# Kernel tuning notes

Hardware: AMD Instinct MI355X
Metric: run time of the kernel (lower is better)

Reference implementation:

```python
import jax, jax.numpy as jnp
import numpy as np

B, L, H, A, M, E, R = 4, 1024, 1024, 16, 128, 32, 992
EMB, BLK, C = 768, 64, 97


def setup_inputs() -> dict:
    key = jax.random.key(0)
    ks = jax.random.split(key, 8)
    return {
        'seq_lhs': jax.random.normal(ks[0], (B, L, H), jnp.float32),
        'ent_lhs': jax.random.normal(ks[1], (B, M, H), jnp.float32),
        'ent_to_seq_attn': jax.random.uniform(ks[2], (B, A, M, L), jnp.float32),
        'mention_entity_ids': jax.random.randint(ks[3], (B, M), 0, E, jnp.int32),
        'hts': jax.random.randint(ks[4], (B, R, 2), 0, E, jnp.int32),
        'head_W': jax.random.normal(ks[5], (2 * H, EMB), jnp.float32) * 0.02,
        'head_b': jnp.zeros((EMB,), jnp.float32),
        'tail_W': jax.random.normal(ks[6], (2 * H, EMB), jnp.float32) * 0.02,
        'tail_b': jnp.zeros((EMB,), jnp.float32),
        'bil_W': jax.random.normal(ks[7], (EMB * BLK, C), jnp.float32) * 0.02,
        'bil_b': jnp.zeros((C,), jnp.float32),
    }


def _pool_doc(seq, ents, attn, ids, ht):
    # seq [L,H], ents [M,H], attn [A,M,L], ids [M], ht [R,2]
    counts = jax.ops.segment_sum(jnp.ones((M,), seq.dtype), ids, num_segments=E)  # [E]
    nz = counts > 0
    # stable segment logsumexp over mentions of each entity (matches torch.logsumexp;
    # single-mention entities reduce to the raw embedding, empty entities -> zeros)
    mx = jax.ops.segment_max(ents, ids, num_segments=E)              # [E,H]
    mx = jnp.where(nz[:, None], mx, 0.0)
    s = jax.ops.segment_sum(jnp.exp(ents - mx[ids]), ids, num_segments=E)
    s = jnp.where(nz[:, None], s, 1.0)
    ent_emb = jnp.where(nz[:, None], mx + jnp.log(s), 0.0)           # [E,H]
    # mean of mention->seq attention per entity (empty -> zeros)
    attn_m = jnp.transpose(attn, (1, 0, 2))                          # [M,A,L]
    asum = jax.ops.segment_sum(attn_m, ids, num_segments=E)          # [E,A,L]
    ent_attn = jnp.where(nz[:, None, None], asum / jnp.maximum(counts, 1.0)[:, None, None], 0.0)
    # gather head/tail entities for each pair
    hs, ts = ent_emb[ht[:, 0]], ent_emb[ht[:, 1]]                    # [R,H]
    ha, ta = ent_attn[ht[:, 0]], ent_attn[ht[:, 1]]                  # [R,A,L]
    w = (ha * ta).mean(axis=1)                                       # [R,L]
    w = w / (w.sum(axis=1, keepdims=True) + 1e-5)
    rel = jnp.einsum('ld,rl->rd', seq, w)                            # [R,H]
    return hs, ts, rel


def reference(seq_lhs, ent_lhs, ent_to_seq_attn, mention_entity_ids, hts,
              head_W, head_b, tail_W, tail_b, bil_W, bil_b):
    hs, ts, rel = jax.vmap(_pool_doc)(seq_lhs, ent_lhs, ent_to_seq_attn,
                                      mention_entity_ids, hts)
    hs = hs.reshape(-1, H)
    ts = ts.reshape(-1, H)
    rel = rel.reshape(-1, H)
    hs = jnp.tanh(jnp.concatenate([hs, rel], axis=1) @ head_W + head_b)  # [N,EMB]
    ts = jnp.tanh(jnp.concatenate([ts, rel], axis=1) @ tail_W + tail_b)
    b1 = hs.reshape(-1, EMB // BLK, BLK)
    b2 = ts.reshape(-1, EMB // BLK, BLK)
    bl = (b1[:, :, :, None] * b2[:, :, None, :]).reshape(-1, EMB * BLK)  # [N,EMB*BLK]
    return bl @ bil_W + bil_b                                            # [N,C]
```

## Files before the change

kernel.cpp:

```cpp
#include <hip/hip_runtime.h>
#include <hip/hip_bf16.h>
#include <math.h>

constexpr int cB   = 4;
constexpr int cL   = 1024;
constexpr int cH   = 1024;
constexpr int cA   = 16;
constexpr int cM   = 128;
constexpr int cE   = 32;
constexpr int cR   = 992;
constexpr int cEMB = 768;
constexpr int cC   = 97;
constexpr int cN   = cB * cR;
constexpr int cNG  = 8;

typedef unsigned short ushort;
typedef __attribute__((ext_vector_type(4))) unsigned short ushort4v;
typedef __attribute__((ext_vector_type(8))) short short8;
typedef __attribute__((ext_vector_type(4))) float float4v;

static __device__ inline float bf2f(ushort u) {
    unsigned v = ((unsigned)u) << 16;
    float f;
    __builtin_memcpy(&f, &v, 4);
    return f;
}
static __device__ inline ushort f2bf(float f) {
    unsigned u;
    __builtin_memcpy(&u, &f, 4);
    unsigned r = (u + 0x7FFFu + ((u >> 16) & 1u)) >> 16;
    return (ushort)r;
}

static __device__ inline void gld16(const ushort* src, ushort* dstbase) {
    __builtin_amdgcn_global_load_lds(
        (const __attribute__((address_space(1))) unsigned int*)src,
        (__attribute__((address_space(3))) unsigned int*)dstbase, 16, 0, 0);
}

__global__ void prep_k(const float* __restrict__ bil_W,
                       const float* __restrict__ head_W,
                       const float* __restrict__ tail_W,
                       const float* __restrict__ seq_lhs,
                       const float* __restrict__ ent_lhs,
                       const int* __restrict__ ids,
                       ushort* __restrict__ Wf,
                       ushort* __restrict__ WTh, ushort* __restrict__ WTt,
                       ushort* __restrict__ seqT,
                       ushort* __restrict__ ent_bf, int* __restrict__ counts) {
    const int id = blockIdx.x;
    const int tid = threadIdx.x;
    __shared__ float tile[32][33];
    __shared__ ushort sWb[64 * 136];
    __shared__ int sid[cM];

    if (id < 768) {
        const int si = id;
        for (int idx = tid; idx < 64 * 128; idx += 256) {
            int r = idx >> 7, c = idx & 127;
            float v = (c < cC) ? bil_W[((size_t)si * 64 + r) * cC + c] : 0.f;
            sWb[r * 136 + c] = f2bf(v);
        }
        __syncthreads();
#pragma unroll
        for (int p = 0; p < 4; p++) {
            int e = tid + p * 256;
            int f = e >> 6, lane = e & 63;
            int g = lane >> 4, col = lane & 15;
            int khalf = f >> 3, ct = f & 7;
            int jb = khalf * 32 + g * 8;
            int c = ct * 16 + col;
            short8 v;
#pragma unroll
            for (int jj = 0; jj < 8; jj++) v[jj] = (short)sWb[(jb + jj) * 136 + c];
            *(short8*)&Wf[(((size_t)si * 16 + f) * 64 + lane) * 8] = v;
        }
    } else if (id < 3840) {
        const int t = id - 768;
        const int bx = t & 63, by = (t >> 6) % 24, bz = t / 1536;
        const float* src = bz ? tail_W : head_W;
        ushort* dst = bz ? WTt : WTh;
        int r0 = bx * 32, c0 = by * 32;
        int tx = tid & 31, ty = tid >> 5;
        for (int p = 0; p < 4; p++) {
            int r = r0 + ty + p * 8, c = c0 + tx;
            tile[ty + p * 8][tx] = src[(size_t)r * cEMB + c];
        }
        __syncthreads();
        for (int p = 0; p < 4; p++) {
            int c = c0 + ty + p * 8, r = r0 + tx;
            dst[(size_t)c * (2 * cH) + r] = f2bf(tile[tx][ty + p * 8]);
        }
    } else if (id < 7936) {
        const int t = id - 3840;
        const int bx = t & 31, by = (t >> 5) & 31, z = t >> 10;
        int r0 = bx * 32, c0 = by * 32;
        int tx = tid & 31, ty = tid >> 5;
        for (int p = 0; p < 4; p++) {
            int r = r0 + ty + p * 8, c = c0 + tx;
            tile[ty + p * 8][tx] = seq_lhs[((size_t)z * cL + r) * cH + c];
        }
        __syncthreads();
        for (int p = 0; p < 4; p++) {
            int c = c0 + ty + p * 8, r = r0 + tx;
            seqT[((size_t)z * cH + c) * cL + r] = f2bf(tile[tx][ty + p * 8]);
        }
    } else {
        const int t = id - 7936;
        const int e = t & 31, b = (t >> 5) & 3, z = t >> 7;
        if (tid < cM) sid[tid] = ids[b * cM + tid];
        __syncthreads();
        int cnt = 0;
        for (int m = 0; m < cM; m++) cnt += (sid[m] == e) ? 1 : 0;
        if (z == 0 && tid == 0) counts[b * cE + e] = cnt;
        int h = z * 256 + tid;
        float mx = -1e30f;
        for (int m = 0; m < cM; m++)
            if (sid[m] == e) mx = fmaxf(mx, ent_lhs[(size_t)(b * cM + m) * cH + h]);
        float s = 0.f;
        for (int m = 0; m < cM; m++)
            if (sid[m] == e) s += __expf(ent_lhs[(size_t)(b * cM + m) * cH + h] - mx);
        ent_bf[(size_t)(b * cE + e) * cH + h] = f2bf((cnt > 0) ? (mx + __logf(s)) : 0.f);
    }
}

__global__ void ent_attn_k(const float* __restrict__ attn, const int* __restrict__ ids,
                           const int* __restrict__ counts, ushort* __restrict__ ent_attn) {
    int ba = blockIdx.x;
    int b = ba / cA, a = ba % cA;
    int tid = threadIdx.x;
    int l = blockIdx.y * 256 + tid;
    __shared__ int sid[cM];
    __shared__ int scnt[cE];
    __shared__ float sacc[256 * 33];
    if (tid < cM) sid[tid] = ids[b * cM + tid];
    if (tid < cE) scnt[tid] = counts[b * cE + tid];
    float* acc = &sacc[tid * 33];
    for (int e2 = 0; e2 < cE; e2++) acc[e2] = 0.f;
    __syncthreads();
    const float* ap = attn + ((size_t)(b * cA + a) * cM) * cL + l;
    for (int m = 0; m < cM; m++) acc[sid[m]] += ap[(size_t)m * cL];
    for (int e2 = 0; e2 < cE; e2++) {
        ent_attn[((size_t)(b * cE + e2) * cA + a) * cL + l] =
            f2bf(acc[e2] / (float)max(scnt[e2], 1));
    }
}

__global__ void w_k(const ushort* __restrict__ ent_attn, const int* __restrict__ hts,
                    ushort* __restrict__ w) {
    int nr = blockIdx.x;
    int b = nr / cR;
    int he = hts[nr * 2 + 0], te = hts[nr * 2 + 1];
    int tid = threadIdx.x;
    int l0 = tid * 4;
    const ushort* ha = ent_attn + ((size_t)(b * cE + he) * cA) * cL + l0;
    const ushort* ta = ent_attn + ((size_t)(b * cE + te) * cA) * cL + l0;
    float v[4] = {0.f, 0.f, 0.f, 0.f};
#pragma unroll
    for (int a = 0; a < cA; a++) {
        ushort4v hv = *(const ushort4v*)&ha[(size_t)a * cL];
        ushort4v tv = *(const ushort4v*)&ta[(size_t)a * cL];
#pragma unroll
        for (int i = 0; i < 4; i++) v[i] += bf2f(hv[i]) * bf2f(tv[i]);
    }
    float psum = 0.f;
#pragma unroll
    for (int i = 0; i < 4; i++) { v[i] *= (1.0f / cA); psum += v[i]; }
    for (int off = 32; off > 0; off >>= 1) psum += __shfl_down(psum, off, 64);
    __shared__ float red[4];
    if ((tid & 63) == 0) red[tid >> 6] = psum;
    __syncthreads();
    float tot = red[0] + red[1] + red[2] + red[3];
    float inv = 1.0f / (tot + 1e-5f);
    ushort4v o;
#pragma unroll
    for (int i = 0; i < 4; i++) o[i] = f2bf(v[i] * inv);
    *(ushort4v*)&w[(size_t)nr * cL + l0] = o;
}

__global__ __launch_bounds__(256) void
rel_mfma2_k(const ushort* __restrict__ wbf, const ushort* __restrict__ seqT,
            ushort* __restrict__ relbf) {
    const int b = blockIdx.z;
    const int h0 = blockIdx.x * 128, r0 = blockIdx.y * 64;
    const int tid = threadIdx.x, lane = tid & 63, wv = tid >> 6;
    const int col = lane & 15, g4 = lane >> 4;
    const int wr = wv >> 1, wc = wv & 1;

    __shared__ ushort sA[2][64 * 64];
    __shared__ ushort sB[2][128 * 64];

    const int lr = lane >> 3;
    const int swz = (lane & 7) ^ lr;

    const int ra0 = wv * 8 + lr, ra1 = ra0 + 32;
    const ushort* a0p = wbf + ((size_t)b * cR + min(r0 + ra0, cR - 1)) * cL + swz * 8;
    const ushort* a1p = wbf + ((size_t)b * cR + min(r0 + ra1, cR - 1)) * cL + swz * 8;
    const ushort* bptr[4];
#pragma unroll
    for (int p = 0; p < 4; p++)
        bptr[p] = seqT + ((size_t)b * cH + h0 + p * 32 + wv * 8 + lr) * cL + swz * 8;

    float4v acc[2][4];
#pragma unroll
    for (int mt = 0; mt < 2; mt++)
#pragma unroll
        for (int ct = 0; ct < 4; ct++) acc[mt][ct] = (float4v){0.f, 0.f, 0.f, 0.f};

#define REL_STAGE(kt, buf) {                                                   \
        gld16(a0p + (kt), &sA[buf][wv * 512]);                                 \
        gld16(a1p + (kt), &sA[buf][(4 + wv) * 512]);                           \
        _Pragma("unroll")                                                      \
        for (int p = 0; p < 4; p++)                                            \
            gld16(bptr[p] + (kt), &sB[buf][(p * 4 + wv) * 512]);               \
    }

    REL_STAGE(0, 0);
    __syncthreads();
    int cur = 0;
    for (int kt = 0; kt < cL; kt += 64) {
        if (kt + 64 < cL) REL_STAGE(kt + 64, cur ^ 1);
#pragma unroll
        for (int k0 = 0; k0 < 64; k0 += 32) {
            short8 av[2];
#pragma unroll
            for (int mt = 0; mt < 2; mt++) {
                int ra = wr * 32 + mt * 16 + col;
                int sg = ((k0 >> 3) + g4) ^ (ra & 7);
                av[mt] = *(const short8*)&sA[cur][ra * 64 + sg * 8];
            }
#pragma unroll
            for (int ct = 0; ct < 4; ct++) {
                int rb = wc * 64 + ct * 16 + col;
                int sg = ((k0 >> 3) + g4) ^ (rb & 7);
                short8 bv = *(const short8*)&sB[cur][rb * 64 + sg * 8];
#pragma unroll
                for (int mt = 0; mt < 2; mt++)
                    acc[mt][ct] = __builtin_amdgcn_mfma_f32_16x16x32_bf16(
                        av[mt], bv, acc[mt][ct], 0, 0, 0);
            }
        }
        __syncthreads();
        cur ^= 1;
    }
#undef REL_STAGE

#pragma unroll
    for (int mt = 0; mt < 2; mt++) {
#pragma unroll
        for (int ct = 0; ct < 4; ct++) {
            int h = h0 + wc * 64 + ct * 16 + col;
            int rowb = r0 + wr * 32 + mt * 16 + g4 * 4;
#pragma unroll
            for (int reg = 0; reg < 4; reg++) {
                int r = rowb + reg;
                if (r < cR)
                    relbf[((size_t)b * cR + r) * cH + h] = f2bf(acc[mt][ct][reg]);
            }
        }
    }
}

__global__ __launch_bounds__(256) void
proj_mfma3_k(const ushort* __restrict__ ent_bf, const ushort* __restrict__ relbf,
             const int* __restrict__ hts,
             const ushort* __restrict__ WTh, const ushort* __restrict__ WTt,
             const float* __restrict__ head_b, const float* __restrict__ tail_b,
             ushort* __restrict__ hsp, ushort* __restrict__ tsp) {
    const int sel = blockIdx.z;
    const ushort* WTp = sel ? WTt : WTh;
    const float* bias = sel ? tail_b : head_b;
    ushort* outp = sel ? tsp : hsp;

    const int e0 = blockIdx.x * 128, n0 = blockIdx.y * 64;
    const int tid = threadIdx.x, lane = tid & 63, wv = tid >> 6;
    const int col = lane & 15, g4 = lane >> 4;
    const int wr = wv >> 1, wc = wv & 1;

    __shared__ ushort sA[2][64 * 64];
    __shared__ ushort sB[2][128 * 64];

    const int lr = lane >> 3;
    const int swz = (lane & 7) ^ lr;

    const int ra0 = wv * 8 + lr, ra1 = ra0 + 32;
    size_t eb0, eb1;
    { int n = n0 + ra0, bb = n / cR; eb0 = ((size_t)(bb * cE + hts[n * 2 + sel])) * cH; }
    { int n = n0 + ra1, bb = n / cR; eb1 = ((size_t)(bb * cE + hts[n * 2 + sel])) * cH; }
    const ushort* aent0 = ent_bf + eb0 + swz * 8;
    const ushort* aent1 = ent_bf + eb1 + swz * 8;
    const ushort* arel0 = relbf + (size_t)(n0 + ra0) * cH + swz * 8;
    const ushort* arel1 = relbf + (size_t)(n0 + ra1) * cH + swz * 8;

    const ushort* bptr[4];
#pragma unroll
    for (int p = 0; p < 4; p++)
        bptr[p] = WTp + (size_t)(e0 + p * 32 + wv * 8 + lr) * (2 * cH) + swz * 8;

    float4v acc[2][4];
#pragma unroll
    for (int mt = 0; mt < 2; mt++)
#pragma unroll
        for (int ct = 0; ct < 4; ct++) acc[mt][ct] = (float4v){0.f, 0.f, 0.f, 0.f};

#define PROJ_STAGE(kt, buf) {                                                  \
        const ushort* a0 = ((kt) < cH) ? aent0 + (kt) : arel0 + ((kt) - cH);   \
        const ushort* a1 = ((kt) < cH) ? aent1 + (kt) : arel1 + ((kt) - cH);   \
        gld16(a0, &sA[buf][wv * 512]);                                         \
        gld16(a1, &sA[buf][(4 + wv) * 512]);                                   \
        _Pragma("unroll")                                                      \
        for (int p = 0; p < 4; p++)                                            \
            gld16(bptr[p] + (kt), &sB[buf][(p * 4 + wv) * 512]);               \
    }

    PROJ_STAGE(0, 0);
    __syncthreads();
    int cur = 0;
    for (int kt = 0; kt < 2 * cH; kt += 64) {
        if (kt + 64 < 2 * cH) PROJ_STAGE(kt + 64, cur ^ 1);
#pragma unroll
        for (int k0 = 0; k0 < 64; k0 += 32) {
            short8 av[2];
#pragma unroll
            for (int mt = 0; mt < 2; mt++) {
                int ra = wr * 32 + mt * 16 + col;
                int sg = ((k0 >> 3) + g4) ^ (ra & 7);
                av[mt] = *(const short8*)&sA[cur][ra * 64 + sg * 8];
            }
#pragma unroll
            for (int ct = 0; ct < 4; ct++) {
                int rb = wc * 64 + ct * 16 + col;
                int sg = ((k0 >> 3) + g4) ^ (rb & 7);
                short8 bv = *(const short8*)&sB[cur][rb * 64 + sg * 8];
#pragma unroll
                for (int mt = 0; mt < 2; mt++)
                    acc[mt][ct] = __builtin_amdgcn_mfma_f32_16x16x32_bf16(
                        av[mt], bv, acc[mt][ct], 0, 0, 0);
            }
        }
        __syncthreads();
        cur ^= 1;
    }
#undef PROJ_STAGE

#pragma unroll
    for (int mt = 0; mt < 2; mt++) {
#pragma unroll
        for (int ct = 0; ct < 4; ct++) {
            int e = e0 + wc * 64 + ct * 16 + col;
            float bv = bias[e];
            int rowb = n0 + wr * 32 + mt * 16 + g4 * 4;
#pragma unroll
            for (int reg = 0; reg < 4; reg++)
                outp[(size_t)(rowb + reg) * cEMB + e] = f2bf(tanhf(acc[mt][ct][reg] + bv));
        }
    }
}

__global__ __launch_bounds__(256) void
bil_mfma13_k(const ushort* __restrict__ hsp, const ushort* __restrict__ tsp,
             const ushort* __restrict__ Wf, float* __restrict__ part) {
    const int grp = blockIdx.x;
    const int n0 = blockIdx.y * 64;
    const int tid = threadIdx.x;
    const int lane = tid & 63, wv = tid >> 6;
    const int col = lane & 15, g4 = lane >> 4;

    __shared__ float sHs[32 * 68];

    float4v acc[4][2];
#pragma unroll
    for (int mt = 0; mt < 4; mt++)
#pragma unroll
        for (int ctl = 0; ctl < 2; ctl++) acc[mt][ctl] = (float4v){0.f, 0.f, 0.f, 0.f};

    const float4v kZero = {0.f, 0.f, 0.f, 0.f};

    const ushort* WfG = Wf + (size_t)grp * 3 * 32 * 8192;
    const ushort* wbase = WfG + ((size_t)(wv * 2) * 64 + lane) * 8;

#define WLOAD(dst, t) {                                                        \
        const ushort* _p = wbase + (size_t)(t) * 8192;                         \
        dst[0][0] = *(const short8*)&_p[0];                                    \
        dst[0][1] = *(const short8*)&_p[512];                                  \
        dst[1][0] = *(const short8*)&_p[4096];                                 \
        dst[1][1] = *(const short8*)&_p[4608];                                 \
    }

#define BILSTEP(ii, w) {                                                       \
        float4v hsv[4];                                                        \
        _Pragma("unroll")                                                      \
        for (int mt = 0; mt < 4; mt++)                                         \
            hsv[mt] = *(const float4v*)&sHs[(ii) * 68 + mt * 16 + g4 * 4];     \
        _Pragma("unroll")                                                      \
        for (int ctl = 0; ctl < 2; ctl++) {                                    \
            _Pragma("unroll")                                                  \
            for (int mt = 0; mt < 4; mt++) {                                   \
                float4v P = __builtin_amdgcn_mfma_f32_16x16x32_bf16(           \
                    tsA[mt][0], w[0][ctl], kZero, 0, 0, 0);                    \
                P = __builtin_amdgcn_mfma_f32_16x16x32_bf16(                   \
                    tsA[mt][1], w[1][ctl], P, 0, 0, 0);                        \
                acc[mt][ctl] += hsv[mt] * P;                                   \
            }                                                                  \
        }                                                                      \
    }

    short8 tsA[4][2];
    short8 wA[2][2], wB[2][2];
    WLOAD(wA, 0);

    for (int s = 0; s < 3; ++s) {
        const int islice = grp * 3 + s;
        const int kb = islice >> 1;

        __syncthreads();
        {
            int row = tid & 63, seg = tid >> 6;
            short8 v = *(const short8*)
                &hsp[(size_t)(n0 + row) * cEMB + islice * 32 + seg * 8];
#pragma unroll
            for (int jj = 0; jj < 8; jj++)
                sHs[(seg * 8 + jj) * 68 + row] = bf2f((ushort)v[jj]);
        }
#pragma unroll
        for (int mt = 0; mt < 4; mt++)
#pragma unroll
            for (int kh = 0; kh < 2; kh++)
                tsA[mt][kh] = *(const short8*)
                    &tsp[(size_t)(n0 + mt * 16 + col) * cEMB
                         + kb * 64 + kh * 32 + g4 * 8];
        __syncthreads();

        for (int i = 0; i < 32; i += 2) {
            const int t = s * 32 + i;
            WLOAD(wB, t + 1);
            BILSTEP(i, wA);
            if (t + 2 < 96) WLOAD(wA, t + 2);
            BILSTEP(i + 1, wB);
        }
    }
#undef WLOAD
#undef BILSTEP

    float* pbase = part + (size_t)grp * cN * 128;
#pragma unroll
    for (int mt = 0; mt < 4; mt++) {
#pragma unroll
        for (int ctl = 0; ctl < 2; ctl++) {
            int c = (wv * 2 + ctl) * 16 + col;
            int rowb = n0 + mt * 16 + g4 * 4;
#pragma unroll
            for (int reg = 0; reg < 4; reg++)
                pbase[(size_t)(rowb + reg) * 128 + c] = acc[mt][ctl][reg];
        }
    }
}

__global__ void bil_reduce_k(const float* __restrict__ part,
                             const float* __restrict__ bil_b,
                             float* __restrict__ out) {
    int n = blockIdx.x;
    int c = threadIdx.x;
    if (c >= cC) return;
    float s = bil_b[c];
#pragma unroll
    for (int g = 0; g < cNG; g++)
        s += part[((size_t)g * cN + n) * 128 + c];
    out[(size_t)n * cC + c] = s;
}

extern "C" void kernel_launch(void* const* d_in, const int* in_sizes, int n_in,
                              void* d_out, int out_size, void* d_ws, size_t ws_size,
                              hipStream_t stream) {
    const float* seq_lhs  = (const float*)d_in[0];
    const float* ent_lhs  = (const float*)d_in[1];
    const float* attn     = (const float*)d_in[2];
    const int*   ids      = (const int*)d_in[3];
    const int*   hts      = (const int*)d_in[4];
    const float* head_W   = (const float*)d_in[5];
    const float* head_b   = (const float*)d_in[6];
    const float* tail_W   = (const float*)d_in[7];
    const float* tail_b   = (const float*)d_in[8];
    const float* bil_W    = (const float*)d_in[9];
    const float* bil_b    = (const float*)d_in[10];
    float* out = (float*)d_out;

    char* ws = (char*)d_ws;
    int*    counts   = (int*)(ws + 0);
    ushort* ent_bf   = (ushort*)(ws + 512);
    ushort* ent_attn = (ushort*)(ws + 262656);
    ushort* wbuf     = (ushort*)(ws + 4456960);
    ushort* relbf    = (ushort*)(ws + 12583424);
    ushort* hsp      = (ushort*)(ws + 20709888);
    ushort* tsp      = (ushort*)(ws + 26804736);
    ushort* Wf       = (ushort*)(ws + 32899584);
    ushort* WTh      = (ushort*)(ws + 45482496);
    ushort* WTt      = (ushort*)(ws + 48628224);
    ushort* seqT     = (ushort*)(ws + 51773952);
    float*  part     = (float*)(ws + 262656);

    hipLaunchKernelGGL(prep_k, dim3(8448), dim3(256), 0, stream,
                       bil_W, head_W, tail_W, seq_lhs, ent_lhs, ids,
                       Wf, WTh, WTt, seqT, ent_bf, counts);
    hipLaunchKernelGGL(ent_attn_k, dim3(cB * cA, cL / 256), dim3(256), 0, stream,
                       attn, ids, counts, ent_attn);
    hipLaunchKernelGGL(w_k, dim3(cN), dim3(256), 0, stream,
                       ent_attn, hts, wbuf);
    hipLaunchKernelGGL(rel_mfma2_k, dim3(cH / 128, 16, cB), dim3(256), 0, stream,
                       wbuf, seqT, relbf);
    hipLaunchKernelGGL(proj_mfma3_k, dim3(cEMB / 128, cN / 64, 2), dim3(256), 0, stream,
                       ent_bf, relbf, hts, WTh, WTt, head_b, tail_b, hsp, tsp);
    hipLaunchKernelGGL(bil_mfma13_k, dim3(cNG, cN / 64), dim3(256), 0, stream,
                       hsp, tsp, Wf, part);
    hipLaunchKernelGGL(bil_reduce_k, dim3(cN), dim3(128), 0, stream,
                       part, bil_b, out);
}
```

Before: 296.3 us.

## Stream bilinear weights through a per-wave LDS ring buffer with async loads

```diff
diff --git a/kernel.cpp b/kernel.cpp
--- a/kernel.cpp
+++ b/kernel.cpp
@@ -358,7 +358,7 @@
 }
 
 __global__ __launch_bounds__(256) void
-bil_mfma13_k(const ushort* __restrict__ hsp, const ushort* __restrict__ tsp,
+bil_mfma15_k(const ushort* __restrict__ hsp, const ushort* __restrict__ tsp,
              const ushort* __restrict__ Wf, float* __restrict__ part) {
     const int grp = blockIdx.x;
     const int n0 = blockIdx.y * 64;
@@ -367,6 +367,7 @@
     const int col = lane & 15, g4 = lane >> 4;
 
     __shared__ float sHs[32 * 68];
+    __shared__ ushort sWr[4][4][2048];
 
     float4v acc[4][2];
 #pragma unroll
@@ -377,37 +378,46 @@
     const float4v kZero = {0.f, 0.f, 0.f, 0.f};
 
     const ushort* WfG = Wf + (size_t)grp * 3 * 32 * 8192;
-    const ushort* wbase = WfG + ((size_t)(wv * 2) * 64 + lane) * 8;
-
-#define WLOAD(dst, t) {                                                        \
-        const ushort* _p = wbase + (size_t)(t) * 8192;                         \
-        dst[0][0] = *(const short8*)&_p[0];                                    \
-        dst[0][1] = *(const short8*)&_p[512];                                  \
-        dst[1][0] = *(const short8*)&_p[4096];                                 \
-        dst[1][1] = *(const short8*)&_p[4608];                                 \
-    }
-
-#define BILSTEP(ii, w) {                                                       \
+    const ushort* srcb = WfG + ((size_t)(wv * 2) * 64 + lane) * 8;
+
+#define WSTAGE(tt, slot) {                                                     \
+        const ushort* _s = srcb + (size_t)(tt) * 8192;                         \
+        gld16(_s,        &sWr[wv][slot][0]);                                   \
+        gld16(_s + 512,  &sWr[wv][slot][512]);                                 \
+        gld16(_s + 4096, &sWr[wv][slot][1024]);                                \
+        gld16(_s + 4608, &sWr[wv][slot][1536]);                                \
+    }
+
+#define BILSTEP15(ii, slot) {                                                  \
+        const ushort* _w = &sWr[wv][slot][lane * 8];                           \
+        short8 w00 = *(const short8*)&_w[0];                     \
+        short8 w01 = *(const short8*)&_w[512];                   \
+        short8 w10 = *(const short8*)&_w[1024];                  \
+        short8 w11 = *(const short8*)&_w[1536];                  \
         float4v hsv[4];                                                        \
         _Pragma("unroll")                                                      \
         for (int mt = 0; mt < 4; mt++)                                         \
             hsv[mt] = *(const float4v*)&sHs[(ii) * 68 + mt * 16 + g4 * 4];     \
         _Pragma("unroll")                                                      \
-        for (int ctl = 0; ctl < 2; ctl++) {                                    \
-            _Pragma("unroll")                                                  \
-            for (int mt = 0; mt < 4; mt++) {                                   \
-                float4v P = __builtin_amdgcn_mfma_f32_16x16x32_bf16(           \
-                    tsA[mt][0], w[0][ctl], kZero, 0, 0, 0);                    \
-                P = __builtin_amdgcn_mfma_f32_16x16x32_bf16(                   \
-                    tsA[mt][1], w[1][ctl], P, 0, 0, 0);                        \
-                acc[mt][ctl] += hsv[mt] * P;                                   \
-            }                                                                  \
+        for (int mt = 0; mt < 4; mt++) {                                       \
+            float4v P = __builtin_amdgcn_mfma_f32_16x16x32_bf16(               \
+                tsA[mt][0], w00, kZero, 0, 0, 0);                              \
+            P = __builtin_amdgcn_mfma_f32_16x16x32_bf16(                       \
+                tsA[mt][1], w10, P, 0, 0, 0);                                  \
+            acc[mt][0] += hsv[mt] * P;                                         \
+            float4v Q = __builtin_amdgcn_mfma_f32_16x16x32_bf16(               \
+                tsA[mt][0], w01, kZero, 0, 0, 0);                              \
+            Q = __builtin_amdgcn_mfma_f32_16x16x32_bf16(                       \
+                tsA[mt][1], w11, Q, 0, 0, 0);                                  \
+            acc[mt][1] += hsv[mt] * Q;                                         \
         }                                                                      \
     }
 
     short8 tsA[4][2];
-    short8 wA[2][2], wB[2][2];
-    WLOAD(wA, 0);
+
+    WSTAGE(0, 0);
+    WSTAGE(1, 1);
+    WSTAGE(2, 2);
 
     for (int s = 0; s < 3; ++s) {
         const int islice = grp * 3 + s;
@@ -431,16 +441,18 @@
                          + kb * 64 + kh * 32 + g4 * 8];
         __syncthreads();
 
-        for (int i = 0; i < 32; i += 2) {
+        for (int i = 0; i < 32; ++i) {
             const int t = s * 32 + i;
-            WLOAD(wB, t + 1);
-            BILSTEP(i, wA);
-            if (t + 2 < 96) WLOAD(wA, t + 2);
-            BILSTEP(i + 1, wB);
-        }
-    }
-#undef WLOAD
-#undef BILSTEP
+            WSTAGE(min(t + 3, 95), (t + 3) & 3);
+            asm volatile("s_waitcnt vmcnt(12)" ::: "memory");
+            __builtin_amdgcn_sched_barrier(0);
+            BILSTEP15(i, t & 3);
+        }
+    }
+#undef WSTAGE
+#undef BILSTEP15
+
+    asm volatile("s_waitcnt vmcnt(0)" ::: "memory");
 
     float* pbase = part + (size_t)grp * cN * 128;
 #pragma unroll
@@ -510,7 +522,7 @@
                        wbuf, seqT, relbf);
     hipLaunchKernelGGL(proj_mfma3_k, dim3(cEMB / 128, cN / 64, 2), dim3(256), 0, stream,
                        ent_bf, relbf, hts, WTh, WTt, head_b, tail_b, hsp, tsp);
-    hipLaunchKernelGGL(bil_mfma13_k, dim3(cNG, cN / 64), dim3(256), 0, stream,
+    hipLaunchKernelGGL(bil_mfma15_k, dim3(cNG, cN / 64), dim3(256), 0, stream,
                        hsp, tsp, Wf, part);
     hipLaunchKernelGGL(bil_reduce_k, dim3(cN), dim3(128), 0, stream,
                        part, bil_b, out);
```

Result: slower. 311.6 us (+5.1%).
